# Optimization experiments

Hardware: AMD Instinct MI355X
Metric: run time of the kernel (lower is better)

Reference implementation:

```python
import jax, jax.numpy as jnp
import numpy as np

NUM_CLUSTERS = 256


def setup_inputs() -> dict:
    key = jax.random.key(0)
    k1, k2, k3 = jax.random.split(key, 3)
    a, b, k = 8192, 8192, NUM_CLUSTERS
    w_mat = jax.random.uniform(k1, (a, b), dtype=jnp.float32)
    # softmax-like assignment probabilities over clusters
    p_l = jax.nn.softmax(jax.random.normal(k2, (a, k), dtype=jnp.float32), axis=-1)
    p_r = jax.nn.softmax(jax.random.normal(k3, (b, k), dtype=jnp.float32), axis=-1)
    clusters_p = jnp.ones((k,), dtype=jnp.float32) / k  # uniform init as in module
    return {"w_mat": w_mat, "p_l": p_l, "p_r": p_r, "clusters_p": clusters_p}


def reference(w_mat, p_l, p_r, clusters_p):
    # Algebraically equivalent to:
    #   ((w[:,:,None] * (p_l[:,None,:] + p_r[None,:,:] - 2*p_l[:,None,:]*p_r[None,:,:]))
    #      .sum((0,1)) / clusters_p).sum()
    # without materializing the (a,b,k) tensor.
    row_w = jnp.sum(w_mat, axis=1)            # (a,)  sum_b w[a,b]
    col_w = jnp.sum(w_mat, axis=0)            # (b,)  sum_a w[a,b]
    rs = row_w @ p_l                           # (k,)  sum_{a,b} w * p_l
    cs = col_w @ p_r                           # (k,)  sum_{a,b} w * p_r
    # cross[k] = sum_{a,b} p_l[a,k] * w[a,b] * p_r[b,k]
    cross = jnp.einsum("ka,ak->k", p_l.T @ w_mat, p_r)  # (k,)
    return jnp.sum((rs + cs - 2.0 * cross) / clusters_p)
```

## Files before the change

kernel.cpp:

```cpp
#include <hip/hip_runtime.h>
#include <stdint.h>

#define A_DIM 8192
#define B_DIM 8192
#define K_CL  256
#define NSLAB 8
#define SLABW (B_DIM / NSLAB)
#define NKS   (SLABW / 64)

typedef short bf16x8 __attribute__((ext_vector_type(8)));
typedef float f32x4  __attribute__((ext_vector_type(4)));
typedef float f32x16 __attribute__((ext_vector_type(16)));
typedef unsigned short u16;

__device__ __forceinline__ u16 f2bf(float f) {
    unsigned int u = __float_as_uint(f);
    u += 0x7fffu + ((u >> 16) & 1u);
    return (u16)(u >> 16);
}

__global__ __launch_bounds__(256) void k_prep(const float* __restrict__ pr,
                                              u16* __restrict__ Bpack,
                                              float* __restrict__ out) {
    const int kb2 = blockIdx.x;
    const int t = threadIdx.x;
    if (kb2 == 0 && t == 0) out[0] = 0.0f;
    const int lane = t & 63, wv = t >> 6;
    const int l31 = lane & 31, half = lane >> 5;
#pragma unroll
    for (int ci = 0; ci < 2; ci++) {
        const int c2 = wv * 2 + ci;
        float v[8];
#pragma unroll
        for (int j = 0; j < 8; j++)
            v[j] = pr[(size_t)(kb2 * 16 + half * 8 + j) * K_CL + c2 * 32 + l31];
        union { bf16x8 b; unsigned int u[4]; } o;
#pragma unroll
        for (int j = 0; j < 4; j++)
            o.u[j] = (unsigned int)f2bf(v[2 * j]) | ((unsigned int)f2bf(v[2 * j + 1]) << 16);
        *(bf16x8*)(Bpack + ((size_t)(kb2 * 8 + c2) * 64 + lane) * 8) = o.b;
    }
}

__global__ __launch_bounds__(256, 2) void k_main(const float* __restrict__ w,
                                                 const float* __restrict__ pl,
                                                 const u16* __restrict__ Bpack,
                                                 const float* __restrict__ cp,
                                                 float* __restrict__ out) {
    __shared__ u16 Abf[4][2][2048];
    __shared__ float rowsum_s[4][32];
    __shared__ float red[4];

    const int bid = blockIdx.x;
    const int slab = bid & 7;
    const int mt  = bid >> 3;
    const int tid = threadIdx.x;
    const int lane = tid & 63, wv = tid >> 6;
    const int l31 = lane & 31, half = lane >> 5;
    const int g4 = lane >> 4, c16 = lane & 15;

    const int m0w = mt * 128 + wv * 32;
    const size_t kbase = (size_t)slab * SLABW;
    const int kb2base = slab * 64;

    const float* wthr = w + (size_t)(m0w + g4) * B_DIM + kbase + c16 * 4;
    u16* lds = &Abf[wv][0][0];
    const int swz = (l31 & 7) << 4;

    f32x16 acc[8];
#pragma unroll
    for (int i = 0; i < 8; i++)
#pragma unroll
        for (int r = 0; r < 16; r++) acc[i][r] = 0.f;
    float sm[8] = {0.f, 0.f, 0.f, 0.f, 0.f, 0.f, 0.f, 0.f};

    f32x4 G[8];
    bf16x8 Bc[8], Bn[8];

#define WAIT8 do { asm volatile("s_waitcnt vmcnt(8)" ::: "memory"); __builtin_amdgcn_sched_barrier(0); } while (0)
#define WAIT0 do { asm volatile("s_waitcnt vmcnt(0)" ::: "memory"); __builtin_amdgcn_sched_barrier(0); } while (0)
#define LGKM0 do { asm volatile("s_waitcnt lgkmcnt(0)" ::: "memory"); __builtin_amdgcn_sched_barrier(0); } while (0)

#define GLOAD(ks) do {                                                                   \
        _Pragma("unroll")                                                                \
        for (int j_ = 0; j_ < 8; j_++)                                                   \
            G[j_] = *(const f32x4*)(wthr + (size_t)(4 * j_) * B_DIM + (size_t)(ks) * 64);\
    } while (0)

#define LOADB(arr, s_, kf_) do {                                                         \
        const u16* bp_ = Bpack + (size_t)(kb2base + (s_) * 4 + (kf_)) * 512 + lane * 8;  \
        _Pragma("unroll")                                                                \
        for (int n2_ = 0; n2_ < 8; n2_++)                                                \
            (arr)[n2_] = *(const bf16x8*)(bp_ + n2_ * 512);                              \
    } while (0)

#define PERM2(hi, lo) __builtin_amdgcn_perm(__float_as_uint(hi), __float_as_uint(lo), 0x07060302u)

#define CONVERT(bufsel) do {                                                             \
        char* lb_ = (char*)lds + (bufsel) * 4096;                                        \
        _Pragma("unroll")                                                                \
        for (int j_ = 0; j_ < 8; j_++) {                                                 \
            sm[j_] += G[j_][0] + G[j_][1] + G[j_][2] + G[j_][3];                         \
            uint2 pj_;                                                                   \
            pj_.x = PERM2(G[j_][1], G[j_][0]);                                           \
            pj_.y = PERM2(G[j_][3], G[j_][2]);                                           \
            *(uint2*)(lb_ + (512 * j_ + 128 * g4)                                        \
                          + ((c16 * 8) ^ (g4 << 4) ^ ((j_ & 1) << 6))) = pj_;            \
        }                                                                                \
    } while (0)

#define KFSTEP(kf_, bufsel, Barr) do {                                                   \
        bf16x8 a_ = *(const bf16x8*)((const char*)lds + (bufsel) * 4096 + l31 * 128      \
                                     + (((kf_) * 32 + half * 16) ^ swz));                \
        __builtin_amdgcn_s_setprio(1);                                                   \
        _Pragma("unroll")                                                                \
        for (int n2_ = 0; n2_ < 8; n2_++)                                                \
            acc[n2_] = __builtin_amdgcn_mfma_f32_32x32x16_bf16(a_, (Barr)[n2_],          \
                                                               acc[n2_], 0, 0, 0);       \
        __builtin_amdgcn_s_setprio(0);                                                   \
    } while (0)

    GLOAD(0);
    WAIT0;
    CONVERT(0);
    GLOAD(1);
    LOADB(Bc, 0, 0);
    LGKM0;

    for (int s = 0; s < NKS - 1; ++s) {
        const int buf = s & 1;
        LOADB(Bn, s, 1);      WAIT8; KFSTEP(0, buf, Bc);
        LOADB(Bc, s, 2);      WAIT8; KFSTEP(1, buf, Bn);
        LOADB(Bn, s, 3);      WAIT8; KFSTEP(2, buf, Bc);
        LOADB(Bc, s + 1, 0);  WAIT8; KFSTEP(3, buf, Bn);
        CONVERT(buf ^ 1);
        if (s < NKS - 2) GLOAD(s + 2);
        LGKM0;
    }
    LOADB(Bn, 15, 1); WAIT8; KFSTEP(0, 1, Bc);
    LOADB(Bc, 15, 2); WAIT8; KFSTEP(1, 1, Bn);
    LOADB(Bn, 15, 3); WAIT8; KFSTEP(2, 1, Bc);
    WAIT0;                   KFSTEP(3, 1, Bn);

#undef KFSTEP
#undef CONVERT
#undef PERM2
#undef LOADB
#undef GLOAD

    {
#pragma unroll
        for (int j = 0; j < 8; j++) {
            float v = sm[j];
            v += __shfl_xor(v, 1, 64);
            v += __shfl_xor(v, 2, 64);
            v += __shfl_xor(v, 4, 64);
            v += __shfl_xor(v, 8, 64);
            if (c16 == 0) rowsum_s[wv][4 * j + g4] = v;
        }
    }
    float rcp_cp[8];
#pragma unroll
    for (int n2 = 0; n2 < 8; n2++)
        rcp_cp[n2] = 1.0f / cp[n2 * 32 + l31];

    float tot = 0.f;
#pragma unroll
    for (int reg = 0; reg < 16; reg++) {
        const int lrow = (reg & 3) + 8 * (reg >> 2) + 4 * half;
        const float rs = rowsum_s[wv][lrow];
        const float* plrow = pl + (size_t)(m0w + lrow) * K_CL + l31;
#pragma unroll
        for (int n2 = 0; n2 < 8; n2++) {
            const float q = acc[n2][reg];
            const float p = plrow[n2 * 32];
            tot += (q + p * (rs - 2.0f * q)) * rcp_cp[n2];
        }
    }
    for (int o = 32; o; o >>= 1) tot += __shfl_down(tot, o, 64);
    if (lane == 0) red[wv] = tot;
    __syncthreads();
    if (tid == 0) atomicAdd(out, red[0] + red[1] + red[2] + red[3]);

#undef WAIT8
#undef WAIT0
#undef LGKM0
}

extern "C" void kernel_launch(void* const* d_in, const int* in_sizes, int n_in,
                              void* d_out, int out_size, void* d_ws, size_t ws_size,
                              hipStream_t stream) {
    const float* w  = (const float*)d_in[0];
    const float* pl = (const float*)d_in[1];
    const float* pr = (const float*)d_in[2];
    const float* cp = (const float*)d_in[3];
    float* out = (float*)d_out;

    u16* Bpack = (u16*)d_ws;

    k_prep<<<dim3(512), dim3(256), 0, stream>>>(pr, Bpack, out);
    k_main<<<dim3(64 * NSLAB), dim3(256), 0, stream>>>(w, pl, Bpack, cp, out);
}
```

Measured before the change: 68.22 us.

## Stage packed B in LDS via async global_load_lds and feed A from registers

Stops giving each wave its own B-fragment register loads and instead streams the packed p_r tile for each k-step into a double-buffered shared LDS buffer using global_load_lds, shared by all four waves with a barrier per step. The w tile is now loaded per lane in the MFMA A-operand layout and converted to bf16 in registers, so the LDS round-trip for A and the swizzled stores go away, and row sums collapse to one shuffle. The aim is to cut redundant global B traffic and VGPR pressure. In exchange it adds a block-wide barrier every step, smaller 32-wide k-steps, and it drops the s_setprio hints.

Result: slower. 73.28 us (+7.4%).

```diff
diff --git a/kernel.cpp b/kernel.cpp
--- a/kernel.cpp
+++ b/kernel.cpp
@@ -5,8 +5,8 @@
 #define B_DIM 8192
 #define K_CL  256
 #define NSLAB 8
-#define SLABW (B_DIM / NSLAB)
-#define NKS   (SLABW / 64)
+#define SLABW 1024
+#define NKS   32
 
 typedef short bf16x8 __attribute__((ext_vector_type(8)));
 typedef float f32x4  __attribute__((ext_vector_type(4)));
@@ -47,122 +47,120 @@
                                                  const u16* __restrict__ Bpack,
                                                  const float* __restrict__ cp,
                                                  float* __restrict__ out) {
-    __shared__ u16 Abf[4][2][2048];
+    __shared__ u16 Bl[2][8192];
     __shared__ float rowsum_s[4][32];
     __shared__ float red[4];
 
     const int bid = blockIdx.x;
     const int slab = bid & 7;
-    const int mt  = bid >> 3;
+    const int m0b = (bid >> 3) * 128;
     const int tid = threadIdx.x;
     const int lane = tid & 63, wv = tid >> 6;
     const int l31 = lane & 31, half = lane >> 5;
-    const int g4 = lane >> 4, c16 = lane & 15;
-
-    const int m0w = mt * 128 + wv * 32;
-    const size_t kbase = (size_t)slab * SLABW;
-    const int kb2base = slab * 64;
-
-    const float* wthr = w + (size_t)(m0w + g4) * B_DIM + kbase + c16 * 4;
-    u16* lds = &Abf[wv][0][0];
-    const int swz = (l31 & 7) << 4;
+    const int m0w = m0b + wv * 32;
+
+    const float* wrow = w + (size_t)(m0w + l31) * B_DIM + slab * SLABW + half * 8;
+    const char* bsrc = (const char*)Bpack + (size_t)slab * 64 * 8192;
 
     f32x16 acc[8];
 #pragma unroll
     for (int i = 0; i < 8; i++)
 #pragma unroll
         for (int r = 0; r < 16; r++) acc[i][r] = 0.f;
-    float sm[8] = {0.f, 0.f, 0.f, 0.f, 0.f, 0.f, 0.f, 0.f};
-
-    f32x4 G[8];
-    bf16x8 Bc[8], Bn[8];
-
-#define WAIT8 do { asm volatile("s_waitcnt vmcnt(8)" ::: "memory"); __builtin_amdgcn_sched_barrier(0); } while (0)
-#define WAIT0 do { asm volatile("s_waitcnt vmcnt(0)" ::: "memory"); __builtin_amdgcn_sched_barrier(0); } while (0)
-#define LGKM0 do { asm volatile("s_waitcnt lgkmcnt(0)" ::: "memory"); __builtin_amdgcn_sched_barrier(0); } while (0)
-
-#define GLOAD(ks) do {                                                                   \
+    float sm = 0.f;
+
+    f32x4 Ga[4], Gb[4];
+
+#define SB0 __builtin_amdgcn_sched_barrier(0)
+#define WAITV(n) do { asm volatile("s_waitcnt vmcnt(" #n ")" ::: "memory"); SB0; } while (0)
+#define BAR do { __builtin_amdgcn_s_barrier(); SB0; } while (0)
+
+#define STAGEB(bufi, s_) do {                                                            \
+        const char* sp_ = bsrc + (size_t)(s_) * 16384 + tid * 16;                        \
+        char* dp_ = (char*)&Bl[(bufi)][0] + tid * 16;                                    \
         _Pragma("unroll")                                                                \
-        for (int j_ = 0; j_ < 8; j_++)                                                   \
-            G[j_] = *(const f32x4*)(wthr + (size_t)(4 * j_) * B_DIM + (size_t)(ks) * 64);\
-    } while (0)
-
-#define LOADB(arr, s_, kf_) do {                                                         \
-        const u16* bp_ = Bpack + (size_t)(kb2base + (s_) * 4 + (kf_)) * 512 + lane * 8;  \
+        for (int j_ = 0; j_ < 4; j_++)                                                   \
+            __builtin_amdgcn_global_load_lds(                                            \
+                (const __attribute__((address_space(1))) void*)(sp_ + j_ * 4096),        \
+                (__attribute__((address_space(3))) void*)(dp_ + j_ * 4096), 16, 0, 0);   \
+        SB0;                                                                             \
+    } while (0)
+
+#define GLOADA(GS, s_) do {                                                              \
+        GS[0] = *(const f32x4*)(wrow + (s_) * 32);                                       \
+        GS[1] = *(const f32x4*)(wrow + (s_) * 32 + 4);                                   \
+        GS[2] = *(const f32x4*)(wrow + (s_) * 32 + 16);                                  \
+        GS[3] = *(const f32x4*)(wrow + (s_) * 32 + 20);                                  \
+        SB0;                                                                             \
+    } while (0)
+
+#define PERM2(hi, lo) __builtin_amdgcn_perm(__float_as_uint(hi), __float_as_uint(lo), 0x07060302u)
+
+#define KF(GS, i0, i1, kf_, lb_) do {                                                    \
+        union { bf16x8 v; unsigned int u[4]; } a_;                                       \
+        a_.u[0] = PERM2(GS[i0][1], GS[i0][0]);                                           \
+        a_.u[1] = PERM2(GS[i0][3], GS[i0][2]);                                           \
+        a_.u[2] = PERM2(GS[i1][1], GS[i1][0]);                                           \
+        a_.u[3] = PERM2(GS[i1][3], GS[i1][2]);                                           \
+        sm += GS[i0][0] + GS[i0][1] + GS[i0][2] + GS[i0][3]                              \
+            + GS[i1][0] + GS[i1][1] + GS[i1][2] + GS[i1][3];                             \
+        const u16* bb_ = (lb_) + (kf_) * 4096 + lane * 8;                                \
         _Pragma("unroll")                                                                \
-        for (int n2_ = 0; n2_ < 8; n2_++)                                                \
-            (arr)[n2_] = *(const bf16x8*)(bp_ + n2_ * 512);                              \
-    } while (0)
-
-#define PERM2(hi, lo) __builtin_amdgcn_perm(__float_as_uint(hi), __float_as_uint(lo), 0x07060302u)
-
-#define CONVERT(bufsel) do {                                                             \
-        char* lb_ = (char*)lds + (bufsel) * 4096;                                        \
-        _Pragma("unroll")                                                                \
-        for (int j_ = 0; j_ < 8; j_++) {                                                 \
-            sm[j_] += G[j_][0] + G[j_][1] + G[j_][2] + G[j_][3];                         \
-            uint2 pj_;                                                                   \
-            pj_.x = PERM2(G[j_][1], G[j_][0]);                                           \
-            pj_.y = PERM2(G[j_][3], G[j_][2]);                                           \
-            *(uint2*)(lb_ + (512 * j_ + 128 * g4)                                        \
-                          + ((c16 * 8) ^ (g4 << 4) ^ ((j_ & 1) << 6))) = pj_;            \
+        for (int c_ = 0; c_ < 8; c_++) {                                                 \
+            bf16x8 bf_ = *(const bf16x8*)(bb_ + c_ * 512);                               \
+            acc[c_] = __builtin_amdgcn_mfma_f32_32x32x16_bf16(a_.v, bf_, acc[c_], 0, 0, 0); \
         }                                                                                \
     } while (0)
 
-#define KFSTEP(kf_, bufsel, Barr) do {                                                   \
-        bf16x8 a_ = *(const bf16x8*)((const char*)lds + (bufsel) * 4096 + l31 * 128      \
-                                     + (((kf_) * 32 + half * 16) ^ swz));                \
-        __builtin_amdgcn_s_setprio(1);                                                   \
-        _Pragma("unroll")                                                                \
-        for (int n2_ = 0; n2_ < 8; n2_++)                                                \
-            acc[n2_] = __builtin_amdgcn_mfma_f32_32x32x16_bf16(a_, (Barr)[n2_],          \
-                                                               acc[n2_], 0, 0, 0);       \
-        __builtin_amdgcn_s_setprio(0);                                                   \
-    } while (0)
-
-    GLOAD(0);
-    WAIT0;
-    CONVERT(0);
-    GLOAD(1);
-    LOADB(Bc, 0, 0);
-    LGKM0;
-
-    for (int s = 0; s < NKS - 1; ++s) {
-        const int buf = s & 1;
-        LOADB(Bn, s, 1);      WAIT8; KFSTEP(0, buf, Bc);
-        LOADB(Bc, s, 2);      WAIT8; KFSTEP(1, buf, Bn);
-        LOADB(Bn, s, 3);      WAIT8; KFSTEP(2, buf, Bc);
-        LOADB(Bc, s + 1, 0);  WAIT8; KFSTEP(3, buf, Bn);
-        CONVERT(buf ^ 1);
-        if (s < NKS - 2) GLOAD(s + 2);
-        LGKM0;
-    }
-    LOADB(Bn, 15, 1); WAIT8; KFSTEP(0, 1, Bc);
-    LOADB(Bc, 15, 2); WAIT8; KFSTEP(1, 1, Bn);
-    LOADB(Bn, 15, 3); WAIT8; KFSTEP(2, 1, Bc);
-    WAIT0;                   KFSTEP(3, 1, Bn);
-
-#undef KFSTEP
-#undef CONVERT
+#define STEP(s_, GC) do {                                                                \
+        STAGEB(((s_) + 1) & 1, (s_) + 1);                                                \
+        const u16* lb_ = &Bl[(s_) & 1][0];                                               \
+        KF(GC, 0, 1, 0, lb_);                                                            \
+        KF(GC, 2, 3, 1, lb_);                                                            \
+        GLOADA(GC, (s_) + 2);                                                            \
+        WAITV(4);                                                                        \
+        BAR;                                                                             \
+    } while (0)
+
+    STAGEB(0, 0);
+    GLOADA(Ga, 0);
+    GLOADA(Gb, 1);
+    WAITV(4);
+    BAR;
+
+    for (int s = 0; s < 30; s += 2) {
+        STEP(s, Ga);
+        STEP(s + 1, Gb);
+    }
+    {
+        STAGEB(1, 31);
+        const u16* lb_ = &Bl[0][0];
+        KF(Ga, 0, 1, 0, lb_);
+        KF(Ga, 2, 3, 1, lb_);
+        WAITV(0);
+        BAR;
+    }
+    {
+        const u16* lb_ = &Bl[1][0];
+        KF(Gb, 0, 1, 0, lb_);
+        KF(Gb, 2, 3, 1, lb_);
+    }
+
+#undef STEP
+#undef KF
 #undef PERM2
-#undef LOADB
-#undef GLOAD
+#undef GLOADA
+#undef STAGEB
 
     {
-#pragma unroll
-        for (int j = 0; j < 8; j++) {
-            float v = sm[j];
-            v += __shfl_xor(v, 1, 64);
-            v += __shfl_xor(v, 2, 64);
-            v += __shfl_xor(v, 4, 64);
-            v += __shfl_xor(v, 8, 64);
-            if (c16 == 0) rowsum_s[wv][4 * j + g4] = v;
-        }
-    }
+        float v = sm + __shfl_xor(sm, 32, 64);
+        if (lane < 32) rowsum_s[wv][l31] = v;
+    }
+
     float rcp_cp[8];
 #pragma unroll
-    for (int n2 = 0; n2 < 8; n2++)
-        rcp_cp[n2] = 1.0f / cp[n2 * 32 + l31];
+    for (int c2 = 0; c2 < 8; c2++)
+        rcp_cp[c2] = 1.0f / cp[c2 * 32 + l31];
 
     float tot = 0.f;
 #pragma unroll
@@ -171,10 +169,10 @@
         const float rs = rowsum_s[wv][lrow];
         const float* plrow = pl + (size_t)(m0w + lrow) * K_CL + l31;
 #pragma unroll
-        for (int n2 = 0; n2 < 8; n2++) {
-            const float q = acc[n2][reg];
-            const float p = plrow[n2 * 32];
-            tot += (q + p * (rs - 2.0f * q)) * rcp_cp[n2];
+        for (int c2 = 0; c2 < 8; c2++) {
+            const float q = acc[c2][reg];
+            const float p = plrow[c2 * 32];
+            tot += (q + p * (rs - 2.0f * q)) * rcp_cp[c2];
         }
     }
     for (int o = 32; o; o >>= 1) tot += __shfl_down(tot, o, 64);
@@ -182,9 +180,9 @@
     __syncthreads();
     if (tid == 0) atomicAdd(out, red[0] + red[1] + red[2] + red[3]);
 
-#undef WAIT8
-#undef WAIT0
-#undef LGKM0
+#undef WAITV
+#undef BAR
+#undef SB0
 }
 
 extern "C" void kernel_launch(void* const* d_in, const int* in_sizes, int n_in,
```
